# Optimization experiments

Hardware: AMD Instinct MI355X
Metric: run time of the kernel (lower is better)

## Reference

```python
import jax, jax.numpy as jnp
import numpy as np

N_NODES = 50000


def gcn_conv(x, W, b, src, dst, num_nodes):
    # x: [N, Fin] -> lin -> [N, Fout]; gather source feats per edge, scatter-add at dst.
    h = x @ W                                   # [N, Fout]
    msg = h[src]                                # [E, Fout]  (message = x_j, no edge_weight)
    out = jax.ops.segment_sum(msg, dst, num_segments=num_nodes)  # [N, Fout]
    return out + b


def setup_inputs() -> dict:
    key = jax.random.key(0)
    k1, k2, k3, k4 = jax.random.split(key, 4)
    x = jax.random.normal(k1, (N_NODES, 128), dtype=jnp.float32)
    edge_index = jax.random.randint(k2, (2, 800000), 0, N_NODES, dtype=jnp.int64)
    W1 = jax.random.normal(k3, (128, 256), dtype=jnp.float32) * (1.0 / np.sqrt(128))
    b1 = jnp.zeros((256,), dtype=jnp.float32)
    W2 = jax.random.normal(k4, (256, 40), dtype=jnp.float32) * (1.0 / np.sqrt(256))
    b2 = jnp.zeros((40,), dtype=jnp.float32)
    return {"x": x, "edge_index": edge_index, "W1": W1, "b1": b1, "W2": W2, "b2": b2}


def reference(x, edge_index, W1, b1, W2, b2):
    src, dst = edge_index[0], edge_index[1]
    h = gcn_conv(x, W1, b1, src, dst, N_NODES)
    h = jax.nn.relu(h)
    out = gcn_conv(h, W2, b2, src, dst, N_NODES)
    return out
```

## Files before the change

### kernel.cpp

```cpp
#include <hip/hip_runtime.h>

typedef unsigned int u32;
typedef unsigned short u16;
using f32x4 = __attribute__((ext_vector_type(4))) float;
using f32x2 = __attribute__((ext_vector_type(2))) float;
using s16x8 = __attribute__((ext_vector_type(8))) short;
using s16x4 = __attribute__((ext_vector_type(4))) short;

__device__ __forceinline__ u16 rne_bf16(float f) {
  u32 u = __float_as_uint(f);
  u += 0x7FFF + ((u >> 16) & 1);
  return (u16)(u >> 16);
}
__device__ __forceinline__ float bf_lo(u32 u) { return __uint_as_float(u << 16); }
__device__ __forceinline__ float bf_hi(u32 u) { return __uint_as_float(u & 0xFFFF0000u); }

#define NBX 12500
#define CAP 64
#define SCAT 2048
#define W1S 72
#define W2S 136

__global__ void zero_k(int4* __restrict__ cnt4, int nc4) {
  int i = blockIdx.x * 256 + threadIdx.x;
  if (i < nc4) cnt4[i] = make_int4(0, 0, 0, 0);
}

__global__ __launch_bounds__(256) void mega_k(const int* __restrict__ srcv,
                                              const int* __restrict__ dstv,
                                              int* __restrict__ cnt,
                                              u16* __restrict__ adj,
                                              int E, int nbin,
                                              const float* __restrict__ x, u32* __restrict__ xb,
                                              int n2,
                                              const float* __restrict__ W1, u16* __restrict__ W1t,
                                              const float* __restrict__ W2, u16* __restrict__ W2t) {
  int b = blockIdx.x, t = threadIdx.x;
  if (b < SCAT) {
    int p = b & 7;
    int lo = p * nbin, hi = lo + nbin;
    int g = b >> 3;
    int ngroups = SCAT >> 3;
    int stride = ngroups * 256;
    for (int i = g * 256 + t; i < E; i += stride) {
      int d = dstv[i];
      if (d >= lo && d < hi) {
        int pos = atomicAdd(&cnt[d], 1);
        if (pos < CAP) adj[(size_t)d * CAP + pos] = (u16)srcv[i];
      }
    }
  } else if (b < SCAT + NBX) {
    int i = (b - SCAT) * 256 + t;
    if (i < n2) {
      f32x2 v = *((const f32x2*)x + i);
      xb[i] = (u32)rne_bf16(v.x) | ((u32)rne_bf16(v.y) << 16);
    }
  } else if (b < SCAT + NBX + 128) {
    int idx = (b - SCAT - NBX) * 256 + t;
    int n = idx >> 7, k = idx & 127;
    W1t[idx] = rne_bf16(W1[k * 256 + n]);
  } else {
    int idx = (b - SCAT - NBX - 128) * 256 + t;
    int c = idx >> 8, k = idx & 255;
    W2t[idx] = (c < 40) ? rne_bf16(W2[k * 40 + c]) : (u16)0;
  }
}

__global__ void agg128_k(const u32* __restrict__ xb, const u16* __restrict__ adj,
                         const int* __restrict__ cnt, u32* __restrict__ aggb, int n) {
  int lane = threadIdx.x & 63;
  int node = blockIdx.x * 4 + (threadIdx.x >> 6);
  if (node >= n) return;
  int deg = cnt[node]; if (deg > CAP) deg = CAP;
  const u16* ab = adj + (size_t)node * CAP;
  float ax = 0.f, ay = 0.f;
  int i = 0;
  for (; i + 8 <= deg; i += 8) {
    u32 u0 = xb[(size_t)ab[i] * 64 + lane];
    u32 u1 = xb[(size_t)ab[i + 1] * 64 + lane];
    u32 u2 = xb[(size_t)ab[i + 2] * 64 + lane];
    u32 u3 = xb[(size_t)ab[i + 3] * 64 + lane];
    u32 u4 = xb[(size_t)ab[i + 4] * 64 + lane];
    u32 u5 = xb[(size_t)ab[i + 5] * 64 + lane];
    u32 u6 = xb[(size_t)ab[i + 6] * 64 + lane];
    u32 u7 = xb[(size_t)ab[i + 7] * 64 + lane];
    ax += ((bf_lo(u0) + bf_lo(u1)) + (bf_lo(u2) + bf_lo(u3)))
        + ((bf_lo(u4) + bf_lo(u5)) + (bf_lo(u6) + bf_lo(u7)));
    ay += ((bf_hi(u0) + bf_hi(u1)) + (bf_hi(u2) + bf_hi(u3)))
        + ((bf_hi(u4) + bf_hi(u5)) + (bf_hi(u6) + bf_hi(u7)));
  }
  for (; i + 2 <= deg; i += 2) {
    u32 u0 = xb[(size_t)ab[i] * 64 + lane];
    u32 u1 = xb[(size_t)ab[i + 1] * 64 + lane];
    ax += bf_lo(u0) + bf_lo(u1); ay += bf_hi(u0) + bf_hi(u1);
  }
  for (; i < deg; ++i) {
    u32 u = xb[(size_t)ab[i] * 64 + lane];
    ax += bf_lo(u); ay += bf_hi(u);
  }
  aggb[(size_t)node * 64 + lane] = (u32)rne_bf16(ax) | ((u32)rne_bf16(ay) << 16);
}

__global__ __launch_bounds__(512) void fused_k(const u16* __restrict__ Ab,
                                               const u16* __restrict__ W1t,
                                               const float* __restrict__ b1,
                                               const u16* __restrict__ W2t,
                                               u32* __restrict__ zb, int M) {
  __shared__ u32 lw1[256 * W1S];
  __shared__ u32 lw2[48 * W2S];
  __shared__ short slab[8][2][16 * 34];
  const int tid = threadIdx.x;
  const int wid = tid >> 6;
  const int l = tid & 63;
  const int p = l & 15, g = l >> 4;
  const int m0 = (blockIdx.x * 8 + wid) * 32;

  s16x8 af[2][4];
  #pragma unroll
  for (int rt = 0; rt < 2; ++rt) {
    int mrow = m0 + rt * 16 + p;
    int mload = (mrow < M) ? mrow : (M - 1);
    const u16* arow = Ab + (size_t)mload * 128 + g * 8;
    #pragma unroll
    for (int kt = 0; kt < 4; ++kt) af[rt][kt] = *(const s16x8*)(arow + kt * 32);
  }

  for (int idx = tid; idx < 16384; idx += 512) {
    int row = idx >> 6, col = idx & 63;
    lw1[row * W1S + col] = ((const u32*)W1t)[idx];
  }
  for (int idx = tid; idx < 6144; idx += 512) {
    int row = idx >> 7, col = idx & 127;
    lw2[row * W2S + col] = ((const u32*)W2t)[idx];
  }
  __syncthreads();

  f32x4 acc2[2][3];
  #pragma unroll
  for (int rt = 0; rt < 2; ++rt)
    #pragma unroll
    for (int n2 = 0; n2 < 3; ++n2) acc2[rt][n2] = (f32x4){0.f, 0.f, 0.f, 0.f};

  #pragma unroll 2
  for (int s = 0; s < 8; ++s) {
    const int n0 = 2 * s, n1 = 2 * s + 1;
    s16x8 wA[4], wB[4], wf[3];
    #pragma unroll
    for (int kt = 0; kt < 4; ++kt) {
      wA[kt] = *(const s16x8*)&lw1[(n0 * 16 + p) * W1S + kt * 16 + g * 4];
      wB[kt] = *(const s16x8*)&lw1[(n1 * 16 + p) * W1S + kt * 16 + g * 4];
    }
    #pragma unroll
    for (int n2 = 0; n2 < 3; ++n2)
      wf[n2] = *(const s16x8*)&lw2[(n2 * 16 + p) * W2S + s * 16 + g * 4];
    float4 bva = *(const float4*)(b1 + n0 * 16 + g * 4);
    float4 bvb = *(const float4*)(b1 + n1 * 16 + g * 4);
    #pragma unroll
    for (int rt = 0; rt < 2; ++rt) {
      f32x4 aA = {0.f, 0.f, 0.f, 0.f};
      f32x4 aB = {0.f, 0.f, 0.f, 0.f};
      #pragma unroll
      for (int kt = 0; kt < 4; ++kt) {
        aA = __builtin_amdgcn_mfma_f32_16x16x32_bf16(wA[kt], af[rt][kt], aA, 0, 0, 0);
        aB = __builtin_amdgcn_mfma_f32_16x16x32_bf16(wB[kt], af[rt][kt], aB, 0, 0, 0);
      }
      s16x4 pa, pb;
      pa[0] = (short)rne_bf16(fmaxf(aA[0] + bva.x, 0.f));
      pa[1] = (short)rne_bf16(fmaxf(aA[1] + bva.y, 0.f));
      pa[2] = (short)rne_bf16(fmaxf(aA[2] + bva.z, 0.f));
      pa[3] = (short)rne_bf16(fmaxf(aA[3] + bva.w, 0.f));
      pb[0] = (short)rne_bf16(fmaxf(aB[0] + bvb.x, 0.f));
      pb[1] = (short)rne_bf16(fmaxf(aB[1] + bvb.y, 0.f));
      pb[2] = (short)rne_bf16(fmaxf(aB[2] + bvb.z, 0.f));
      pb[3] = (short)rne_bf16(fmaxf(aB[3] + bvb.w, 0.f));
      *(s16x4*)&slab[wid][rt][p * 34 + g * 4] = pa;
      *(s16x4*)&slab[wid][rt][p * 34 + 16 + g * 4] = pb;
    }
    #pragma unroll
    for (int n2 = 0; n2 < 3; ++n2) {
      #pragma unroll
      for (int rt = 0; rt < 2; ++rt) {
        s16x8 a2 = *(const s16x8*)&slab[wid][rt][p * 34 + g * 8];
        acc2[rt][n2] = __builtin_amdgcn_mfma_f32_16x16x32_bf16(wf[n2], a2, acc2[rt][n2], 0, 0, 0);
      }
    }
  }

  #pragma unroll
  for (int rt = 0; rt < 2; ++rt) {
    int mrow = m0 + rt * 16 + p;
    if (mrow < M) {
      #pragma unroll
      for (int n2 = 0; n2 < 3; ++n2) {
        int c0 = n2 * 16 + g * 4;
        if (c0 < 40) {
          uint2 o;
          o.x = (u32)rne_bf16(acc2[rt][n2][0]) | ((u32)rne_bf16(acc2[rt][n2][1]) << 16);
          o.y = (u32)rne_bf16(acc2[rt][n2][2]) | ((u32)rne_bf16(acc2[rt][n2][3]) << 16);
          *(uint2*)(zb + (size_t)mrow * 20 + n2 * 8 + g * 2) = o;
        }
      }
    }
  }
}

__global__ void agg40_k(const u32* __restrict__ zb, const u16* __restrict__ adj,
                        const int* __restrict__ cnt, const float* __restrict__ bias,
                        float* __restrict__ outp, int n) {
  int hl = threadIdx.x & 31;
  int node = blockIdx.x * 8 + (threadIdx.x >> 5);
  if (node >= n || hl >= 20) return;
  int deg = cnt[node]; if (deg > CAP) deg = CAP;
  const u16* ab = adj + (size_t)node * CAP;
  float ax = 0.f, ay = 0.f;
  int i = 0;
  for (; i + 4 <= deg; i += 4) {
    u32 u0 = zb[(size_t)ab[i] * 20 + hl];
    u32 u1 = zb[(size_t)ab[i + 1] * 20 + hl];
    u32 u2 = zb[(size_t)ab[i + 2] * 20 + hl];
    u32 u3 = zb[(size_t)ab[i + 3] * 20 + hl];
    ax += (bf_lo(u0) + bf_lo(u1)) + (bf_lo(u2) + bf_lo(u3));
    ay += (bf_hi(u0) + bf_hi(u1)) + (bf_hi(u2) + bf_hi(u3));
  }
  for (; i < deg; ++i) {
    u32 u = zb[(size_t)ab[i] * 20 + hl];
    ax += bf_lo(u); ay += bf_hi(u);
  }
  float2 bv = ((const float2*)bias)[hl];
  ((float2*)(outp + (size_t)node * 40))[hl] = make_float2(ax + bv.x, ay + bv.y);
}

extern "C" void kernel_launch(void* const* d_in, const int* in_sizes, int n_in,
                              void* d_out, int out_size, void* d_ws, size_t ws_size,
                              hipStream_t stream) {
  const float* x  = (const float*)d_in[0];
  const int*   ei = (const int*)d_in[1];
  const float* W1 = (const float*)d_in[2];
  const float* b1 = (const float*)d_in[3];
  const float* W2 = (const float*)d_in[4];
  const float* b2 = (const float*)d_in[5];
  float* out = (float*)d_out;

  int N = in_sizes[0] / 128;
  int E = in_sizes[1] / 2;
  const int* src = ei;
  const int* dst = ei + E;

  char* ws = (char*)d_ws;
  size_t off = 0;
  auto carve = [&](size_t bytes) {
    char* p = ws + off;
    off += (bytes + 255) & ~(size_t)255;
    return p;
  };
  u32* xb    = (u32*)carve((size_t)N * 128 * 2);
  u32* aggb  = (u32*)carve((size_t)N * 128 * 2);
  u16* W1t   = (u16*)carve(256 * 128 * 2);
  u16* W2t   = (u16*)carve(48 * 256 * 2);
  u32* zbuf  = (u32*)carve((size_t)N * 20 * 4);
  int* cnt   = (int*)carve((size_t)N * 4);
  u16* adj   = (u16*)carve((size_t)N * CAP * 2);

  int nbin = (N + 7) / 8;
  int nc4 = (N + 3) / 4;

  zero_k<<<(nc4 + 255) / 256, 256, 0, stream>>>((int4*)cnt, nc4);
  mega_k<<<SCAT + NBX + 128 + 48, 256, 0, stream>>>(src, dst, cnt, adj, E, nbin,
                                                    x, xb, N * 64, W1, W1t, W2, W2t);
  agg128_k<<<(N + 3) / 4, 256, 0, stream>>>(xb, adj, cnt, aggb, N);
  fused_k<<<(N + 255) / 256, 512, 0, stream>>>((const u16*)aggb, W1t, b1, W2t, zbuf, N);
  agg40_k<<<(N + 7) / 8, 256, 0, stream>>>(zbuf, adj, cnt, b2, out, N);
}
```

Baseline: 119.1 us.

## Split bf16 features into four column slabs to localize gather working set

The bf16 copy of x is stored as four column-major slabs of 32 features each. The first aggregation kernel now processes one slab at a time across all nodes, with 16 lanes per node. Each gather pass then touches a 3.2 MB slab that can stay resident in L2 or the infinity cache, instead of scattered 256-byte rows across 12.8 MB. The cost is 64-byte gathers per neighbor, four reads of each adjacency list, and partial-row writes to the aggregate.

```diff
diff --git a/kernel.cpp b/kernel.cpp
--- a/kernel.cpp
+++ b/kernel.cpp
@@ -31,8 +31,8 @@
                                               int* __restrict__ cnt,
                                               u16* __restrict__ adj,
                                               int E, int nbin,
-                                              const float* __restrict__ x, u32* __restrict__ xb,
-                                              int n2,
+                                              const float* __restrict__ x, u32* __restrict__ xbs,
+                                              int n2, int n16,
                                               const float* __restrict__ W1, u16* __restrict__ W1t,
                                               const float* __restrict__ W2, u16* __restrict__ W2t) {
   int b = blockIdx.x, t = threadIdx.x;
@@ -53,7 +53,10 @@
     int i = (b - SCAT) * 256 + t;
     if (i < n2) {
       f32x2 v = *((const f32x2*)x + i);
-      xb[i] = (u32)rne_bf16(v.x) | ((u32)rne_bf16(v.y) << 16);
+      u32 pk = (u32)rne_bf16(v.x) | ((u32)rne_bf16(v.y) << 16);
+      int node = i >> 6, col = i & 63;
+      int s = col >> 4, c = col & 15;
+      xbs[(size_t)s * n16 + node * 16 + c] = pk;
     }
   } else if (b < SCAT + NBX + 128) {
     int idx = (b - SCAT - NBX) * 256 + t;
@@ -66,39 +69,44 @@
   }
 }
 
-__global__ void agg128_k(const u32* __restrict__ xb, const u16* __restrict__ adj,
-                         const int* __restrict__ cnt, u32* __restrict__ aggb, int n) {
-  int lane = threadIdx.x & 63;
-  int node = blockIdx.x * 4 + (threadIdx.x >> 6);
+__global__ __launch_bounds__(256) void agg128_k(const u32* __restrict__ xbs,
+                                                const u16* __restrict__ adj,
+                                                const int* __restrict__ cnt,
+                                                u32* __restrict__ aggb, int n, int n16, int nbp) {
+  int f = blockIdx.x / nbp;
+  int nb = blockIdx.x % nbp;
+  int sg = threadIdx.x >> 4, c = threadIdx.x & 15;
+  int node = nb * 16 + sg;
   if (node >= n) return;
   int deg = cnt[node]; if (deg > CAP) deg = CAP;
   const u16* ab = adj + (size_t)node * CAP;
+  const u32* base = xbs + (size_t)f * n16 + c;
   float ax = 0.f, ay = 0.f;
   int i = 0;
   for (; i + 8 <= deg; i += 8) {
-    u32 u0 = xb[(size_t)ab[i] * 64 + lane];
-    u32 u1 = xb[(size_t)ab[i + 1] * 64 + lane];
-    u32 u2 = xb[(size_t)ab[i + 2] * 64 + lane];
-    u32 u3 = xb[(size_t)ab[i + 3] * 64 + lane];
-    u32 u4 = xb[(size_t)ab[i + 4] * 64 + lane];
-    u32 u5 = xb[(size_t)ab[i + 5] * 64 + lane];
-    u32 u6 = xb[(size_t)ab[i + 6] * 64 + lane];
-    u32 u7 = xb[(size_t)ab[i + 7] * 64 + lane];
+    u32 u0 = base[(size_t)ab[i] * 16];
+    u32 u1 = base[(size_t)ab[i + 1] * 16];
+    u32 u2 = base[(size_t)ab[i + 2] * 16];
+    u32 u3 = base[(size_t)ab[i + 3] * 16];
+    u32 u4 = base[(size_t)ab[i + 4] * 16];
+    u32 u5 = base[(size_t)ab[i + 5] * 16];
+    u32 u6 = base[(size_t)ab[i + 6] * 16];
+    u32 u7 = base[(size_t)ab[i + 7] * 16];
     ax += ((bf_lo(u0) + bf_lo(u1)) + (bf_lo(u2) + bf_lo(u3)))
         + ((bf_lo(u4) + bf_lo(u5)) + (bf_lo(u6) + bf_lo(u7)));
     ay += ((bf_hi(u0) + bf_hi(u1)) + (bf_hi(u2) + bf_hi(u3)))
         + ((bf_hi(u4) + bf_hi(u5)) + (bf_hi(u6) + bf_hi(u7)));
   }
   for (; i + 2 <= deg; i += 2) {
-    u32 u0 = xb[(size_t)ab[i] * 64 + lane];
-    u32 u1 = xb[(size_t)ab[i + 1] * 64 + lane];
+    u32 u0 = base[(size_t)ab[i] * 16];
+    u32 u1 = base[(size_t)ab[i + 1] * 16];
     ax += bf_lo(u0) + bf_lo(u1); ay += bf_hi(u0) + bf_hi(u1);
   }
   for (; i < deg; ++i) {
-    u32 u = xb[(size_t)ab[i] * 64 + lane];
+    u32 u = base[(size_t)ab[i] * 16];
     ax += bf_lo(u); ay += bf_hi(u);
   }
-  aggb[(size_t)node * 64 + lane] = (u32)rne_bf16(ax) | ((u32)rne_bf16(ay) << 16);
+  aggb[(size_t)node * 64 + f * 16 + c] = (u32)rne_bf16(ax) | ((u32)rne_bf16(ay) << 16);
 }
 
 __global__ __launch_bounds__(512) void fused_k(const u16* __restrict__ Ab,
@@ -253,7 +261,7 @@
     off += (bytes + 255) & ~(size_t)255;
     return p;
   };
-  u32* xb    = (u32*)carve((size_t)N * 128 * 2);
+  u32* xbs   = (u32*)carve((size_t)N * 128 * 2);
   u32* aggb  = (u32*)carve((size_t)N * 128 * 2);
   u16* W1t   = (u16*)carve(256 * 128 * 2);
   u16* W2t   = (u16*)carve(48 * 256 * 2);
@@ -263,11 +271,12 @@
 
   int nbin = (N + 7) / 8;
   int nc4 = (N + 3) / 4;
+  int nbp = (N + 15) / 16;
 
   zero_k<<<(nc4 + 255) / 256, 256, 0, stream>>>((int4*)cnt, nc4);
   mega_k<<<SCAT + NBX + 128 + 48, 256, 0, stream>>>(src, dst, cnt, adj, E, nbin,
-                                                    x, xb, N * 64, W1, W1t, W2, W2t);
-  agg128_k<<<(N + 3) / 4, 256, 0, stream>>>(xb, adj, cnt, aggb, N);
+                                                    x, xbs, N * 64, N * 16, W1, W1t, W2, W2t);
+  agg128_k<<<4 * nbp, 256, 0, stream>>>(xbs, adj, cnt, aggb, N, N * 16, nbp);
   fused_k<<<(N + 255) / 256, 512, 0, stream>>>((const u16*)aggb, W1t, b1, W2t, zbuf, N);
   agg40_k<<<(N + 7) / 8, 256, 0, stream>>>(zbuf, adj, cnt, b2, out, N);
 }
```

After: 126.8 us. 1.06x slower.
